# Kernel optimization log

Measured on AMD Instinct MI355X. Metric: run time of the kernel, lower is better.

The kernel has to match this reference:

```python
import jax, jax.numpy as jnp
import numpy as np
from jax import lax

B, N, D = 8, 4096, 64
RATIO = 0.25
S = int(N * RATIO)  # 1024 sampled centroids
RADII = (0.1, 0.2, 0.4)
KS = (16, 32, 128)
MLPS = ((32, 32, 64), (64, 64, 128), (64, 96, 128))


def setup_inputs() -> dict:
    key = jax.random.key(0)
    ks = jax.random.split(key, 11)
    inp = {
        "xyz": jax.random.uniform(ks[0], (B, N, 3), dtype=jnp.float32),
        "features": jax.random.normal(ks[1], (B, N, D), dtype=jnp.float32),
    }
    c = 2
    for i, mlp in enumerate(MLPS):
        cin = D + 3  # in_channel + 3 prepended as in __init__
        for j, cout in enumerate(mlp):
            inp[f"w{i}_{j}"] = jax.random.normal(ks[c], (cout, cin), dtype=jnp.float32) * 0.02
            inp[f"b{i}_{j}"] = jnp.zeros((cout,), jnp.float32)
            c += 1
            cin = cout
    return inp


def fps(xyz, n_samples):
    # iterative farthest point sampling, vectorized over batch
    b, n, _ = xyz.shape

    def body(carry, _):
        dist, farthest = carry                                # [B,N], [B]
        centroid = xyz[jnp.arange(b), farthest]               # [B,3]
        d = jnp.sum((xyz - centroid[:, None, :]) ** 2, -1)    # [B,N]
        dist = jnp.minimum(dist, d)
        nxt = jnp.argmax(dist, -1).astype(jnp.int32)
        return (dist, nxt), farthest

    init = (jnp.full((b, n), 1e10, xyz.dtype), jnp.zeros((b,), jnp.int32))
    _, idxs = lax.scan(body, init, None, length=n_samples)    # [S,B]
    idxs = idxs.T                                             # [B,S]
    return jnp.take_along_axis(xyz, idxs[..., None], axis=1)  # [B,S,3]


def ball_group(xyz, new_xyz, features, radius, k):
    # ball query: up to k neighbors of each centroid within radius
    b, n, _ = xyz.shape
    s = new_xyz.shape[1]
    sqd = (jnp.sum(new_xyz ** 2, -1)[:, :, None]
           + jnp.sum(xyz ** 2, -1)[:, None, :]
           - 2.0 * jnp.einsum('bsc,bnc->bsn', new_xyz, xyz))   # [B,S,N]
    idx = jnp.broadcast_to(jnp.arange(n, dtype=jnp.int32), (b, s, n))
    idx = jnp.where(sqd > radius * radius, n, idx)
    idx = jnp.sort(idx, axis=-1)[:, :, :k]                     # [B,S,K]
    first = idx[:, :, :1]
    idx = jnp.where(idx == n, first, idx)                      # pad with first neighbor

    def gather(pts):
        return jnp.take_along_axis(pts, idx.reshape(b, s * k, 1), axis=1).reshape(b, s, k, pts.shape[-1])

    g_xyz = gather(xyz) - new_xyz[:, :, None, :]               # recentered offsets
    g_feat = gather(features)
    return jnp.concatenate([g_xyz, g_feat], axis=-1)           # [B,S,K,3+D]


def _forward(xyz, features, params):
    new_xyz = fps(xyz, S)
    outs = []
    for radius, k, layers in zip(RADII, KS, params):
        g = ball_group(xyz, new_xyz, features, radius, k)
        for w, bias in layers:  # 1x1 Conv2d == pointwise matmul, then ReLU
            g = jax.nn.relu(jnp.einsum('bskc,oc->bsko', g, w) + bias)
        outs.append(jnp.max(g, axis=2))                        # max-pool over K -> [B,S,Cout]
    return new_xyz, jnp.concatenate(outs, axis=-1)             # [B,S,3], [B,S,320]


def reference(xyz, features,
              w0_0, b0_0, w0_1, b0_1, w0_2, b0_2,
              w1_0, b1_0, w1_1, b1_1, w1_2, b1_2,
              w2_0, b2_0, w2_1, b2_1, w2_2, b2_2):
    params = [[(w0_0, b0_0), (w0_1, b0_1), (w0_2, b0_2)],
              [(w1_0, b1_0), (w1_1, b1_1), (w1_2, b1_2)],
              [(w2_0, b2_0), (w2_1, b2_1), (w2_2, b2_2)]]
    return _forward(xyz, features, params)
```

## Files before the change

### kernel.cpp

```cpp
#include <hip/hip_runtime.h>

#define NB   8
#define NPTS 4096
#define NS   1024
#define NF   64

typedef __bf16 bf16x8 __attribute__((ext_vector_type(8)));
typedef float  f32x4  __attribute__((ext_vector_type(4)));

struct WPrep {
  const float* src[9];
  int CO[9], CI[9], KC[9], off[9];
};

__global__ __launch_bounds__(256) void wprep_kernel(WPrep a, __bf16* __restrict__ dst) {
  const int id = blockIdx.y;
  const int t  = blockIdx.x * 256 + threadIdx.x;
  const int CT = a.CO[id] >> 4;
  const int KC = a.KC[id], CI = a.CI[id];
  if (t >= CT * KC * 64) return;
  const int lane = t & 63;
  const int fidx = t >> 6;
  const int kc = fidx % KC;
  const int ct = fidx / KC;
  const int n  = ct * 16 + (lane & 15);
  const int k0 = kc * 32 + (lane >> 4) * 8;
  const float* src = a.src[id];
  __bf16* d = dst + a.off[id] + (size_t)t * 8;
#pragma unroll
  for (int j = 0; j < 8; ++j) {
    const int k = k0 + j;
    d[j] = (__bf16)((k < CI) ? src[n * CI + k] : 0.0f);
  }
}

__global__ __launch_bounds__(256) void fps_kernel(const float* __restrict__ xyz,
                                                  float* __restrict__ new_xyz) {
  const int b   = blockIdx.x;
  const int tid = threadIdx.x;
  __shared__ float sx[NPTS], sy[NPTS], sz[NPTS];
  __shared__ unsigned long long keys[8];

  const float* xb = xyz + (size_t)b * NPTS * 3;
  for (int p = tid; p < NPTS; p += 256) {
    sx[p] = xb[p * 3 + 0];
    sy[p] = xb[p * 3 + 1];
    sz[p] = xb[p * 3 + 2];
  }
  __syncthreads();

  float px[16], py[16], pz[16], dist[16];
#pragma unroll
  for (int r = 0; r < 16; ++r) {
    const int p = tid + 256 * r;
    px[r] = sx[p]; py[r] = sy[p]; pz[r] = sz[p];
    dist[r] = 1e10f;
  }

  const int wid = tid >> 6;
  int far = 0;
  for (int j = 0; j < NS; ++j) {
    const float cx = sx[far], cy = sy[far], cz = sz[far];
    if (tid == 0) {
      float* o = new_xyz + ((size_t)b * NS + j) * 3;
      o[0] = cx; o[1] = cy; o[2] = cz;
    }
    float bv = -1.0f;
    int   bi = 0;
#pragma unroll
    for (int r = 0; r < 16; ++r) {
      const float dx = __fsub_rn(px[r], cx);
      const float dy = __fsub_rn(py[r], cy);
      const float dz = __fsub_rn(pz[r], cz);
      const float d  = __fadd_rn(__fadd_rn(__fmul_rn(dx, dx), __fmul_rn(dy, dy)),
                                 __fmul_rn(dz, dz));
      const float nd = fminf(dist[r], d);
      dist[r] = nd;
      if (nd > bv) { bv = nd; bi = tid + 256 * r; }
    }
    unsigned long long key =
        ((unsigned long long)__float_as_uint(bv) << 32) | (unsigned)(~bi);
#pragma unroll
    for (int off = 1; off < 64; off <<= 1) {
      const unsigned long long ok = __shfl_xor(key, off);
      if (ok > key) key = ok;
    }
    const int par = (j & 1) * 4;
    if ((tid & 63) == 0) keys[par + wid] = key;
    __syncthreads();
    unsigned long long k0 = keys[par + 0];
    const unsigned long long k1 = keys[par + 1];
    const unsigned long long k2 = keys[par + 2];
    const unsigned long long k3 = keys[par + 3];
    if (k1 > k0) k0 = k1;
    if (k2 > k0) k0 = k2;
    if (k3 > k0) k0 = k3;
    far = (int)(~(unsigned)k0) & 0xFFF;
  }
}

__global__ __launch_bounds__(64) void group_kernel(
    const float* __restrict__ xyz, const float* __restrict__ new_xyz,
    int* __restrict__ nbr0, int* __restrict__ nbr1, int* __restrict__ nbr2,
    int* __restrict__ cnt0, int* __restrict__ cnt1, int* __restrict__ cnt2) {
  const int bs   = blockIdx.x;
  const int b    = bs >> 10;
  const int lane = threadIdx.x;
  const float r2_0 = (float)(0.1 * 0.1);
  const float r2_1 = (float)(0.2 * 0.2);
  const float r2_2 = (float)(0.4 * 0.4);

  const float cx = new_xyz[bs * 3 + 0];
  const float cy = new_xyz[bs * 3 + 1];
  const float cz = new_xyz[bs * 3 + 2];
  const float sn = __fadd_rn(__fadd_rn(__fmul_rn(cx, cx), __fmul_rn(cy, cy)),
                             __fmul_rn(cz, cz));
  const float* xb = xyz + (size_t)b * NPTS * 3;
  const unsigned long long below = (1ull << lane) - 1ull;

  int c0 = 0, c1 = 0, c2 = 0;
  for (int base = 0; base < NPTS; base += 64) {
    const int p = base + lane;
    const float x = xb[p * 3 + 0], y = xb[p * 3 + 1], z = xb[p * 3 + 2];
    const float sp = __fadd_rn(__fadd_rn(__fmul_rn(x, x), __fmul_rn(y, y)),
                               __fmul_rn(z, z));
    const float dt = __fadd_rn(__fadd_rn(__fmul_rn(cx, x), __fmul_rn(cy, y)),
                               __fmul_rn(cz, z));
    const float sqd = __fsub_rn(__fadd_rn(sn, sp), __fmul_rn(2.0f, dt));
    const bool in0 = (sqd <= r2_0);
    const bool in1 = (sqd <= r2_1);
    const bool in2 = (sqd <= r2_2);
    const unsigned long long m0 = __ballot(in0);
    const unsigned long long m1 = __ballot(in1);
    const unsigned long long m2 = __ballot(in2);
    if (c0 < 16) {
      const int slot = c0 + __popcll(m0 & below);
      if (in0 && slot < 16) nbr0[bs * 16 + slot] = p;
      c0 = min(c0 + __popcll(m0), 16);
    }
    if (c1 < 32) {
      const int slot = c1 + __popcll(m1 & below);
      if (in1 && slot < 32) nbr1[bs * 32 + slot] = p;
      c1 = min(c1 + __popcll(m1), 32);
    }
    if (c2 < 128) {
      const int slot = c2 + __popcll(m2 & below);
      if (in2 && slot < 128) nbr2[bs * 128 + slot] = p;
      c2 = min(c2 + __popcll(m2), 128);
    }
    if (c0 == 16 && c1 == 32 && c2 == 128) break;
  }
  if (lane == 0) {
    cnt0[bs] = c0;
    cnt1[bs] = c1;
    cnt2[bs] = c2;
  }
}

template <int RT, int KC, int CO, int SIN, int SOUT, bool LAST>
__device__ __forceinline__ void wave_layer(const __bf16* in, __bf16* outb,
                                           const __bf16* __restrict__ wf,
                                           const float* __restrict__ bias,
                                           int lane, float* colmax) {
  bf16x8 a[RT][KC];
#pragma unroll
  for (int rt = 0; rt < RT; ++rt)
#pragma unroll
    for (int kc = 0; kc < KC; ++kc)
      a[rt][kc] = *(const bf16x8*)(in + (rt * 16 + (lane & 15)) * SIN + kc * 32 +
                                   (lane >> 4) * 8);
#pragma unroll
  for (int ct = 0; ct < CO / 16; ++ct) {
    const float bv = bias[ct * 16 + (lane & 15)];
    bf16x8 bfr[KC];
#pragma unroll
    for (int kc = 0; kc < KC; ++kc)
      bfr[kc] = *(const bf16x8*)(wf + ((size_t)(ct * KC + kc) * 64 + lane) * 8);
    float cm = 0.0f;
#pragma unroll
    for (int rt = 0; rt < RT; ++rt) {
      f32x4 acc = {0.0f, 0.0f, 0.0f, 0.0f};
#pragma unroll
      for (int kc = 0; kc < KC; ++kc)
        acc = __builtin_amdgcn_mfma_f32_16x16x32_bf16(a[rt][kc], bfr[kc], acc, 0, 0, 0);
      if constexpr (!LAST) {
#pragma unroll
        for (int r = 0; r < 4; ++r) {
          const int row = rt * 16 + (lane >> 4) * 4 + r;
          const float v = fmaxf(acc[r] + bv, 0.0f);
          outb[row * SOUT + ct * 16 + (lane & 15)] = (__bf16)v;
        }
      } else {
#pragma unroll
        for (int r = 0; r < 4; ++r) cm = fmaxf(cm, acc[r] + bv);
      }
    }
    if constexpr (LAST) colmax[ct] = fmaxf(colmax[ct], cm);
  }
}

template <int K, int C1, int C2, int C3, int WPP, int PPB>
__global__ __launch_bounds__(64 * WPP * PPB) void mlp_mfma(
    const float* __restrict__ xyz, const float* __restrict__ feat,
    const float* __restrict__ new_xyz,
    const int* __restrict__ nbr, const int* __restrict__ cnt_arr,
    const __bf16* __restrict__ wf1, const float* __restrict__ b1,
    const __bf16* __restrict__ wf2, const float* __restrict__ b2,
    const __bf16* __restrict__ wf3, const float* __restrict__ b3,
    float* __restrict__ out, int ch_off) {
  constexpr int SX  = 104;
  constexpr int SH1 = C1 + 8;
  constexpr int SH2 = C2 + 8;
  constexpr int KC1 = 3;
  constexpr int KC2 = C1 / 32;
  constexpr int KC3 = C2 / 32;
  constexpr int PT  = (104 + SH1) * K;
  constexpr int MW  = K / WPP;
  constexpr int RT  = MW / 16;
  static_assert(WPP == 1 || SH2 == SX, "h2 overlay must match X rows for WPP>1");
  __shared__ __bf16 lds[PPB * PT];
  __shared__ float  red[(WPP > 1) ? WPP * C3 : 1];

  const int tid  = threadIdx.x;
  const int lane = tid & 63;
  const int wid  = tid >> 6;

  constexpr int TPN = (64 * WPP) / K;
  constexpr int FPT = NF / TPN;
  {
    const int ln = tid / TPN;
    const int s  = tid - ln * TPN;
    const int lp = ln / K;
    const int n  = ln - lp * K;
    const int p  = blockIdx.x * PPB + lp;
    const int b  = p >> 10;
    const int cnt = cnt_arr[p];
    const int idx = nbr[p * K + min(n, cnt - 1)];
    __bf16* Xr = lds + lp * PT + n * SX;
    const float4* fp4 = (const float4*)(feat + ((size_t)b * NPTS + idx) * NF + s * FPT);
#pragma unroll
    for (int j = 0; j < FPT / 4; ++j) {
      const float4 v = fp4[j];
      Xr[3 + s * FPT + 4 * j + 0] = (__bf16)v.x;
      Xr[3 + s * FPT + 4 * j + 1] = (__bf16)v.y;
      Xr[3 + s * FPT + 4 * j + 2] = (__bf16)v.z;
      Xr[3 + s * FPT + 4 * j + 3] = (__bf16)v.w;
    }
    if (s == 0) {
      const float* xp = xyz + ((size_t)b * NPTS + idx) * 3;
      Xr[0] = (__bf16)(xp[0] - new_xyz[p * 3 + 0]);
      Xr[1] = (__bf16)(xp[1] - new_xyz[p * 3 + 1]);
      Xr[2] = (__bf16)(xp[2] - new_xyz[p * 3 + 2]);
#pragma unroll
      for (int k = 67; k < 96; ++k) Xr[k] = (__bf16)0.0f;
    }
  }

  const int lpg = wid / WPP;
  const int wv  = wid - lpg * WPP;
  const int p   = blockIdx.x * PPB + lpg;
  const __bf16* X  = lds + lpg * PT + wv * MW * SX;
  __bf16*       H1 = lds + lpg * PT + K * 104 + wv * MW * SH1;
  __bf16*       H2 = lds + lpg * PT + wv * MW * SH2;

  float colmax[C3 / 16];
#pragma unroll
  for (int ct = 0; ct < C3 / 16; ++ct) colmax[ct] = 0.0f;

  wave_layer<RT, KC1, C1, SX, SH1, false>(X, H1, wf1, b1, lane, nullptr);
  wave_layer<RT, KC2, C2, SH1, SH2, false>(H1, H2, wf2, b2, lane, nullptr);
  wave_layer<RT, KC3, C3, SH2, 0, true>(H2, nullptr, wf3, b3, lane, colmax);

#pragma unroll
  for (int ct = 0; ct < C3 / 16; ++ct) {
    float v = colmax[ct];
    v = fmaxf(v, __shfl_xor(v, 16));
    v = fmaxf(v, __shfl_xor(v, 32));
    colmax[ct] = v;
  }

  if constexpr (WPP == 1) {
    if (lane < 16) {
      float* op = out + (size_t)p * 320 + ch_off;
#pragma unroll
      for (int ct = 0; ct < C3 / 16; ++ct) op[ct * 16 + lane] = colmax[ct];
    }
  } else {
    if (lane < 16) {
#pragma unroll
      for (int ct = 0; ct < C3 / 16; ++ct)
        red[wv * C3 + ct * 16 + lane] = colmax[ct];
    }
    __syncthreads();
    if (tid < C3) {
      float v = red[tid];
#pragma unroll
      for (int w = 1; w < WPP; ++w) v = fmaxf(v, red[w * C3 + tid]);
      out[(size_t)p * 320 + ch_off + tid] = v;
    }
  }
}

extern "C" void kernel_launch(void* const* d_in, const int* in_sizes, int n_in,
                              void* d_out, int out_size, void* d_ws, size_t ws_size,
                              hipStream_t stream) {
  const float* xyz  = (const float*)d_in[0];
  const float* feat = (const float*)d_in[1];
  float* out      = (float*)d_out;
  float* new_xyz  = out;
  float* feat_out = out + 24576;

  __bf16* wsb = (__bf16*)d_ws;
  int*    wsi = (int*)d_ws;

  const int OW[9] = {0, 3072, 4096, 6144, 12288, 16384, 24576, 30720, 36864};
  const int widx[9] = {2, 4, 6, 8, 10, 12, 14, 16, 18};
  const int co[9] = {32, 32, 64, 64, 64, 128, 64, 96, 128};
  const int ci[9] = {67, 32, 32, 67, 64, 64, 67, 64, 96};
  const int kc[9] = {3, 1, 1, 3, 2, 2, 3, 2, 3};
  WPrep wp;
  for (int i = 0; i < 9; ++i) {
    wp.src[i] = (const float*)d_in[widx[i]];
    wp.CO[i] = co[i]; wp.CI[i] = ci[i]; wp.KC[i] = kc[i]; wp.off[i] = OW[i];
  }
  wprep_kernel<<<dim3(6, 9), 256, 0, stream>>>(wp, wsb);

  fps_kernel<<<NB, 256, 0, stream>>>(xyz, new_xyz);

  int* cnt0 = wsi + 24576;
  int* cnt1 = wsi + 32768;
  int* cnt2 = wsi + 40960;
  int* nbr0 = wsi + 49152;
  int* nbr1 = wsi + 180224;
  int* nbr2 = wsi + 442368;
  group_kernel<<<NB * NS, 64, 0, stream>>>(xyz, new_xyz, nbr0, nbr1, nbr2,
                                           cnt0, cnt1, cnt2);

  mlp_mfma<16, 32, 32, 64, 1, 4><<<NB * NS / 4, 256, 0, stream>>>(
      xyz, feat, new_xyz, nbr0, cnt0,
      wsb + OW[0], (const float*)d_in[3],
      wsb + OW[1], (const float*)d_in[5],
      wsb + OW[2], (const float*)d_in[7],
      feat_out, 0);
  mlp_mfma<32, 64, 64, 128, 1, 2><<<NB * NS / 2, 128, 0, stream>>>(
      xyz, feat, new_xyz, nbr1, cnt1,
      wsb + OW[3], (const float*)d_in[9],
      wsb + OW[4], (const float*)d_in[11],
      wsb + OW[5], (const float*)d_in[13],
      feat_out, 64);
  mlp_mfma<128, 64, 96, 128, 4, 1><<<NB * NS, 256, 0, stream>>>(
      xyz, feat, new_xyz, nbr2, cnt2,
      wsb + OW[6], (const float*)d_in[15],
      wsb + OW[7], (const float*)d_in[17],
      wsb + OW[8], (const float*)d_in[19],
      feat_out, 192);
}
```

Before: 1.018 ms.

## Speed up FPS argmax with DPP float reduction and 512-thread blocks

The farthest-point-sampling kernel now runs 512 threads per batch with 8 contiguous points per thread instead of 256 threads with 16 strided points. The per-wavefront argmax moves from a six-step 64-bit shuffle reduction to a DPP float max, a readlane and a ballot that picks the first lane holding the max. Contiguous point ownership keeps the lowest-index tie-break correct. The aim is to shorten the serial per-iteration reduction latency that dominates FPS, at the cost of combining 8 wave keys per iteration instead of 4.

```diff
diff --git a/kernel.cpp b/kernel.cpp
--- a/kernel.cpp
+++ b/kernel.cpp
@@ -34,30 +34,37 @@
   }
 }
 
-__global__ __launch_bounds__(256) void fps_kernel(const float* __restrict__ xyz,
+template <int CTRL>
+__device__ __forceinline__ float dpp_fmax_step(float v) {
+  const int t = __builtin_amdgcn_update_dpp(0, __float_as_int(v), CTRL, 0xf, 0xf, true);
+  return fmaxf(v, __int_as_float(t));
+}
+
+__global__ __launch_bounds__(512) void fps_kernel(const float* __restrict__ xyz,
                                                   float* __restrict__ new_xyz) {
   const int b   = blockIdx.x;
   const int tid = threadIdx.x;
   __shared__ float sx[NPTS], sy[NPTS], sz[NPTS];
-  __shared__ unsigned long long keys[8];
+  __shared__ alignas(16) unsigned long long keys[16];
 
   const float* xb = xyz + (size_t)b * NPTS * 3;
-  for (int p = tid; p < NPTS; p += 256) {
+  for (int p = tid; p < NPTS; p += 512) {
     sx[p] = xb[p * 3 + 0];
     sy[p] = xb[p * 3 + 1];
     sz[p] = xb[p * 3 + 2];
   }
   __syncthreads();
 
-  float px[16], py[16], pz[16], dist[16];
-#pragma unroll
-  for (int r = 0; r < 16; ++r) {
-    const int p = tid + 256 * r;
+  float px[8], py[8], pz[8], dist[8];
+#pragma unroll
+  for (int r = 0; r < 8; ++r) {
+    const int p = tid * 8 + r;
     px[r] = sx[p]; py[r] = sy[p]; pz[r] = sz[p];
     dist[r] = 1e10f;
   }
 
-  const int wid = tid >> 6;
+  const int wid  = tid >> 6;
+  const int lane = tid & 63;
   int far = 0;
   for (int j = 0; j < NS; ++j) {
     const float cx = sx[far], cy = sy[far], cz = sz[far];
@@ -68,7 +75,7 @@
     float bv = -1.0f;
     int   bi = 0;
 #pragma unroll
-    for (int r = 0; r < 16; ++r) {
+    for (int r = 0; r < 8; ++r) {
       const float dx = __fsub_rn(px[r], cx);
       const float dy = __fsub_rn(py[r], cy);
       const float dz = __fsub_rn(pz[r], cz);
@@ -76,26 +83,32 @@
                                  __fmul_rn(dz, dz));
       const float nd = fminf(dist[r], d);
       dist[r] = nd;
-      if (nd > bv) { bv = nd; bi = tid + 256 * r; }
-    }
-    unsigned long long key =
-        ((unsigned long long)__float_as_uint(bv) << 32) | (unsigned)(~bi);
-#pragma unroll
-    for (int off = 1; off < 64; off <<= 1) {
-      const unsigned long long ok = __shfl_xor(key, off);
-      if (ok > key) key = ok;
-    }
-    const int par = (j & 1) * 4;
-    if ((tid & 63) == 0) keys[par + wid] = key;
+      if (nd > bv) { bv = nd; bi = tid * 8 + r; }
+    }
+    float v = bv;
+    v = dpp_fmax_step<0x111>(v);
+    v = dpp_fmax_step<0x112>(v);
+    v = dpp_fmax_step<0x114>(v);
+    v = dpp_fmax_step<0x118>(v);
+    v = dpp_fmax_step<0x142>(v);
+    v = dpp_fmax_step<0x143>(v);
+    const float wmax = __int_as_float(
+        __builtin_amdgcn_readlane(__float_as_int(v), 63));
+    const unsigned long long cand = __ballot(bv == wmax);
+    const int fl = (int)__ffsll((long long)cand) - 1;
+    const int par = (j & 1) * 8;
+    if (lane == fl)
+      keys[par + wid] = ((unsigned long long)__float_as_uint(wmax) << 32) |
+                        (unsigned)(~bi);
     __syncthreads();
-    unsigned long long k0 = keys[par + 0];
-    const unsigned long long k1 = keys[par + 1];
-    const unsigned long long k2 = keys[par + 2];
-    const unsigned long long k3 = keys[par + 3];
-    if (k1 > k0) k0 = k1;
-    if (k2 > k0) k0 = k2;
-    if (k3 > k0) k0 = k3;
-    far = (int)(~(unsigned)k0) & 0xFFF;
+    const unsigned long long* kk = keys + par;
+    unsigned long long k = kk[0];
+#pragma unroll
+    for (int i = 1; i < 8; ++i) {
+      const unsigned long long o = kk[i];
+      if (o > k) k = o;
+    }
+    far = (int)(~(unsigned)k) & 0xFFF;
   }
 }
 
@@ -325,7 +338,7 @@
   }
   wprep_kernel<<<dim3(6, 9), 256, 0, stream>>>(wp, wsb);
 
-  fps_kernel<<<NB, 256, 0, stream>>>(xyz, new_xyz);
+  fps_kernel<<<NB, 512, 0, stream>>>(xyz, new_xyz);
 
   int* cnt0 = wsi + 24576;
   int* cnt1 = wsi + 32768;
```

After: 893.1 us. 12.3% less time.
